# Optimization experiments

Hardware: AMD Instinct MI355X
Metric: run time of the kernel (lower is better)

The kernel has to match this reference:

```python
import jax, jax.numpy as jnp
import numpy as np

B, H, W, C = 16, 32, 32, 512
HEADS, DHEAD = 8, 64  # head * channel == C
GROUPS, EPS = 32, 1e-5


def setup_inputs() -> dict:
    key = jax.random.key(0)
    ks = jax.random.split(key, 6)
    return {
        "x": jax.random.normal(ks[0], (B, H, W, C), jnp.float32),
        "gn_gamma": jnp.ones((C,), jnp.float32),
        "gn_beta": jnp.zeros((C,), jnp.float32),
        "wq": jax.random.normal(ks[1], (C, HEADS * DHEAD), jnp.float32) * 0.02,
        "wk": jax.random.normal(ks[2], (C, HEADS * DHEAD), jnp.float32) * 0.02,
        "wv": jax.random.normal(ks[3], (C, HEADS * DHEAD), jnp.float32) * 0.02,
        "conv_w": jax.random.normal(ks[4], (3, 3, HEADS * DHEAD, C), jnp.float32) * 0.02,
        "conv_b": jnp.zeros((C,), jnp.float32),
    }


def _group_norm(x, gamma, beta):
    b, h, w, c = x.shape
    xg = x.reshape(b, h, w, GROUPS, c // GROUPS)
    mean = jnp.mean(xg, axis=(1, 2, 4), keepdims=True)
    var = jnp.var(xg, axis=(1, 2, 4), keepdims=True)
    xn = (xg - mean) * jax.lax.rsqrt(var + EPS)
    return xn.reshape(b, h, w, c) * gamma + beta


def reference(x, gn_gamma, gn_beta, wq, wk, wv, conv_w, conv_b):
    xn = _group_norm(x, gn_gamma, gn_beta)          # [B,H,W,C]
    t = xn.reshape(B, H * W, C)                      # tokens [B,S,C]
    q = (t @ wq).reshape(B, H * W, HEADS, DHEAD)
    k = (t @ wk).reshape(B, H * W, HEADS, DHEAD)
    v = (t @ wv).reshape(B, H * W, HEADS, DHEAD)
    scale = 1.0 / jnp.sqrt(jnp.asarray(DHEAD, q.dtype))
    scores = jnp.einsum("bqhd,bkhd->bhqk", q, k) * scale  # [B,HEADS,S,S]
    weights = jax.nn.softmax(scores, axis=-1)
    out = jnp.einsum("bhqk,bkhd->bqhd", weights, v)       # [B,S,HEADS,DHEAD]
    out = out.reshape(B, H, W, HEADS * DHEAD)
    y = jax.lax.conv_general_dilated(
        out, conv_w, window_strides=(1, 1), padding=((1, 1), (1, 1)),
        dimension_numbers=("NHWC", "HWIO", "NHWC")) + conv_b
    return y + x
```

## Files before the change

kernel.cpp:

```cpp
#include <hip/hip_runtime.h>
#include <hip/hip_bf16.h>

#define Bn 16
#define Cc 512
#define Ss 1024
#define HEADS 8
#define DHEAD 64
#define GROUPS 32
#define CPG 16
#define EPSv 1e-5f
#define Mtok (Bn*Ss)
#define QKVS 1536
#define PROW 34
#define PIMG (PROW*PROW)

typedef __hip_bfloat16 bf16;
typedef __attribute__((ext_vector_type(8))) short short8;
typedef __attribute__((ext_vector_type(4))) float f32x4;

union U4 { uint4 u; bf16 h[8]; };
union B4 { ushort4 u; bf16 h[4]; };

__device__ __forceinline__ void stage16(const bf16* g, bf16* l) {
    __builtin_amdgcn_global_load_lds((const __attribute__((address_space(1))) void*)g,
                                     (__attribute__((address_space(3))) void*)l,
                                     16, 0, 0);
}

__global__ __launch_bounds__(256) void wtrans(const float* __restrict__ src,
                                              bf16* __restrict__ dst) {
    size_t off = (size_t)blockIdx.y * 262144;
    int t = blockIdx.x * 256 + threadIdx.x;
    int n = t & 511, k8 = (t >> 9) * 8;
    const float* s = src + off + (size_t)k8 * 512 + n;
    U4 o;
#pragma unroll
    for (int j = 0; j < 8; j++) o.h[j] = __float2bfloat16(s[(size_t)j * 512]);
    *(uint4*)(dst + off + (size_t)n * 512 + k8) = o.u;
}

__global__ __launch_bounds__(256) void gn_stats(const float* __restrict__ x,
                                                float* __restrict__ stats) {
    int bg = blockIdx.x;
    int b = bg >> 5, g = bg & 31;
    int tid = threadIdx.x;
    const size_t base = (size_t)b * Ss * Cc + g * CPG;
    float sum = 0.f, sq = 0.f;
    for (int i = tid; i < 4096; i += 256) {
        int s = i >> 2, c4 = (i & 3) * 4;
        float4 t = *(const float4*)(x + base + (size_t)s * Cc + c4);
        sum += t.x + t.y + t.z + t.w;
        sq  += t.x * t.x + t.y * t.y + t.z * t.z + t.w * t.w;
    }
    __shared__ float s1[4], s2[4];
#pragma unroll
    for (int off = 32; off > 0; off >>= 1) {
        sum += __shfl_down(sum, off);
        sq  += __shfl_down(sq,  off);
    }
    if ((tid & 63) == 0) { s1[tid >> 6] = sum; s2[tid >> 6] = sq; }
    __syncthreads();
    if (tid == 0) {
        float S = s1[0] + s1[1] + s1[2] + s1[3];
        float Q = s2[0] + s2[1] + s2[2] + s2[3];
        float mean = S * (1.f / 16384.f);
        float var  = Q * (1.f / 16384.f) - mean * mean;
        stats[bg * 2 + 0] = mean;
        stats[bg * 2 + 1] = rsqrtf(var + EPSv);
    }
}

__global__ __launch_bounds__(256) void gn_apply(const float* __restrict__ x,
                                                const float* __restrict__ stats,
                                                const float* __restrict__ gamma,
                                                const float* __restrict__ beta,
                                                bf16* __restrict__ xn) {
    size_t i = (size_t)blockIdx.x * 256 + threadIdx.x;
    size_t e = i * 4;
    int c0 = (int)(e & (Cc - 1));
    int token = (int)(e >> 9);
    int b = token >> 10;
    int g = c0 >> 4;
    float mean = stats[(b * 32 + g) * 2 + 0];
    float rstd = stats[(b * 32 + g) * 2 + 1];
    float4 t  = *(const float4*)(x + e);
    float4 gm = *(const float4*)(gamma + c0);
    float4 bt = *(const float4*)(beta + c0);
    B4 o;
    o.h[0] = __float2bfloat16((t.x - mean) * rstd * gm.x + bt.x);
    o.h[1] = __float2bfloat16((t.y - mean) * rstd * gm.y + bt.y);
    o.h[2] = __float2bfloat16((t.z - mean) * rstd * gm.z + bt.z);
    o.h[3] = __float2bfloat16((t.w - mean) * rstd * gm.w + bt.w);
    *(ushort4*)(xn + e) = o.u;
}

__global__ __launch_bounds__(256) void zero_pad(bf16* __restrict__ Pad) {
    int idx = blockIdx.x * 256 + threadIdx.x;
    int b = idx / (132 * 64);
    int rem = idx - b * 132 * 64;
    int t = rem >> 6, seg = rem & 63;
    int r, c;
    if (t < 34)      { r = 0;  c = t; }
    else if (t < 68) { r = 33; c = t - 34; }
    else { int u = t - 68; r = 1 + (u >> 1); c = (u & 1) * 33; }
    uint4 z = {0u, 0u, 0u, 0u};
    *(uint4*)(Pad + ((size_t)b * PIMG + r * PROW + c) * Cc + seg * 8) = z;
}

__global__ __launch_bounds__(256) void gemm_qkv(const bf16* __restrict__ A,
                                                const bf16* __restrict__ Wt,
                                                bf16* __restrict__ C) {
    __shared__ __align__(16) bf16 As[128][32];
    __shared__ __align__(16) bf16 Bs[128][32];
    int tid = threadIdx.x;
    int wave = tid >> 6, lane = tid & 63;
    int l15 = lane & 15, quad = lane >> 4;
    int wm = wave >> 1, wn = wave & 1;
    int m0 = blockIdx.y * 128, n0 = blockIdx.x * 128;
    int lr = lane >> 2, kseg = (lane & 3) * 8;
    int ar0 = wave * 32 + lr;

    const bf16* ga = A  + (size_t)(m0 + ar0) * Cc + kseg;
    const bf16* gb = Wt + (size_t)(n0 + ar0) * Cc + kseg;
    bf16* la0 = &As[wave * 32][0];
    bf16* la1 = &As[wave * 32 + 16][0];
    bf16* lb0 = &Bs[wave * 32][0];
    bf16* lb1 = &Bs[wave * 32 + 16][0];

    f32x4 acc[4][4] = {};
    for (int k0 = 0; k0 < 512; k0 += 32) {
        __syncthreads();
        stage16(ga + k0,                  la0);
        stage16(ga + k0 + (size_t)16 * Cc, la1);
        stage16(gb + k0,                  lb0);
        stage16(gb + k0 + (size_t)16 * Cc, lb1);
        __syncthreads();
        short8 af[4], bfv[4];
#pragma unroll
        for (int mt = 0; mt < 4; mt++) af[mt]  = *(const short8*)&As[wm * 64 + mt * 16 + l15][quad * 8];
#pragma unroll
        for (int nt = 0; nt < 4; nt++) bfv[nt] = *(const short8*)&Bs[wn * 64 + nt * 16 + l15][quad * 8];
#pragma unroll
        for (int mt = 0; mt < 4; mt++)
#pragma unroll
            for (int nt = 0; nt < 4; nt++)
                acc[mt][nt] = __builtin_amdgcn_mfma_f32_16x16x32_bf16(af[mt], bfv[nt], acc[mt][nt], 0, 0, 0);
    }
#pragma unroll
    for (int mt = 0; mt < 4; mt++)
#pragma unroll
        for (int r = 0; r < 4; r++) {
            size_t row = (size_t)(m0 + wm * 64 + mt * 16 + quad * 4 + r) * QKVS + n0 + wn * 64 + l15;
#pragma unroll
            for (int nt = 0; nt < 4; nt++)
                C[row + nt * 16] = __float2bfloat16(acc[mt][nt][r]);
        }
}

__global__ __launch_bounds__(256) void attention_mfma(const bf16* __restrict__ QKV,
                                                      bf16* __restrict__ Pad) {
    int blk = blockIdx.x;
    int qt = blk & 15;
    int bh = blk >> 4;
    int h = bh & (HEADS - 1), b = bh >> 3;
    int tid = threadIdx.x;
    int wave = tid >> 6, lane = tid & 63;
    int l15 = lane & 15, quad = lane >> 4;

    __shared__ __align__(16) bf16 Ks[2][32][72];
    __shared__ __align__(16) bf16 Vt[2][64][40];
    __shared__ __align__(16) bf16 Ps[4][16][40];

    const size_t base = (size_t)b * Ss * QKVS + h * DHEAD;
    const bf16* kbase = QKV + base + 512;
    const bf16* vbase = QKV + base + 1024;

    int q0 = qt * 64 + wave * 16;
    const bf16* qrow = QKV + base + (size_t)(q0 + l15) * QKVS + quad * 8;
    short8 qf0 = *(const short8*)(qrow);
    short8 qf1 = *(const short8*)(qrow + 32);

    f32x4 oacc[4] = {{0.f,0.f,0.f,0.f},{0.f,0.f,0.f,0.f},{0.f,0.f,0.f,0.f},{0.f,0.f,0.f,0.f}};
    float lsum[4] = {0.f, 0.f, 0.f, 0.f};
    const f32x4 zero4 = {0.f, 0.f, 0.f, 0.f};

    int tok = tid & 31, d0 = (tid >> 5) * 8;

    uint4 nk, nv;
    {
        const size_t rb = (size_t)tok * QKVS + d0;
        nk = *(const uint4*)(kbase + rb);
        nv = *(const uint4*)(vbase + rb);
    }
    *(uint4*)&Ks[0][tok][d0] = nk;
    { U4 u; u.u = nv;
#pragma unroll
      for (int i = 0; i < 8; i++) Vt[0][d0 + i][tok] = u.h[i]; }
    __syncthreads();

    for (int c = 0; c < 32; ++c) {
        int buf = c & 1;
        if (c + 1 < 32) {
            const size_t rb = (size_t)((c + 1) * 32 + tok) * QKVS + d0;
            nk = *(const uint4*)(kbase + rb);
            nv = *(const uint4*)(vbase + rb);
        }
#pragma unroll
        for (int kg = 0; kg < 2; kg++) {
            short8 kf0 = *(const short8*)&Ks[buf][kg * 16 + l15][quad * 8];
            short8 kf1 = *(const short8*)&Ks[buf][kg * 16 + l15][32 + quad * 8];
            f32x4 s = __builtin_amdgcn_mfma_f32_16x16x32_bf16(qf0, kf0, zero4, 0, 0, 0);
            s = __builtin_amdgcn_mfma_f32_16x16x32_bf16(qf1, kf1, s, 0, 0, 0);
#pragma unroll
            for (int r = 0; r < 4; r++) {
                float p = __expf(s[r] * 0.125f);
                lsum[r] += p;
                Ps[wave][quad * 4 + r][kg * 16 + l15] = __float2bfloat16(p);
            }
        }
        short8 pf = *(const short8*)&Ps[wave][l15][quad * 8];
#pragma unroll
        for (int dt = 0; dt < 4; dt++) {
            short8 vf = *(const short8*)&Vt[buf][dt * 16 + l15][quad * 8];
            oacc[dt] = __builtin_amdgcn_mfma_f32_16x16x32_bf16(pf, vf, oacc[dt], 0, 0, 0);
        }
        if (c + 1 < 32) {
            *(uint4*)&Ks[buf ^ 1][tok][d0] = nk;
            U4 u; u.u = nv;
#pragma unroll
            for (int i = 0; i < 8; i++) Vt[buf ^ 1][d0 + i][tok] = u.h[i];
        }
        __syncthreads();
    }

#pragma unroll
    for (int r = 0; r < 4; r++) {
#pragma unroll
        for (int m = 1; m < 16; m <<= 1) lsum[r] += __shfl_xor(lsum[r], m);
    }
#pragma unroll
    for (int r = 0; r < 4; r++) {
        float inv = 1.f / lsum[r];
        int s = q0 + quad * 4 + r;
        size_t rowoff = ((size_t)(b * PROW + (s >> 5) + 1) * PROW + (s & 31) + 1) * Cc + h * DHEAD;
#pragma unroll
        for (int dt = 0; dt < 4; dt++)
            Pad[rowoff + dt * 16 + l15] = __float2bfloat16(oacc[dt][r] * inv);
    }
}

__global__ __launch_bounds__(256) void conv_mfma(const bf16* __restrict__ Pad,
                                                 const bf16* __restrict__ Wct,
                                                 const float* __restrict__ bias,
                                                 const float* __restrict__ xres,
                                                 float* __restrict__ out) {
    __shared__ __align__(16) bf16 As[128][32];
    __shared__ __align__(16) bf16 Bs[128][32];
    int tid = threadIdx.x;
    int wave = tid >> 6, lane = tid & 63;
    int l15 = lane & 15, quad = lane >> 4;
    int wm = wave >> 1, wn = wave & 1;
    int m0 = blockIdx.y * 128, n0 = blockIdx.x * 128;
    int lr = lane >> 2, kseg = (lane & 3) * 8;
    int ar0 = wave * 32 + lr;

    int tok = m0 + ar0;
    int b = tok >> 10, oh = (tok & 1023) >> 5, ow = tok & 31;
    int prow = (b * PROW + oh + 1) * PROW + ow + 1;

    const bf16* gb = Wct + (size_t)(n0 + ar0) * Cc + kseg;
    bf16* la0 = &As[wave * 32][0];
    bf16* la1 = &As[wave * 32 + 16][0];
    bf16* lb0 = &Bs[wave * 32][0];
    bf16* lb1 = &Bs[wave * 32 + 16][0];

    f32x4 acc[4][4] = {};
    for (int tap = 0; tap < 9; ++tap) {
        int dy = tap / 3 - 1, dx = tap % 3 - 1;
        const bf16* ga = Pad + (size_t)(prow + dy * PROW + dx) * Cc + kseg;
        const bf16* gw = gb + (size_t)tap * (Cc * Cc);
        for (int k0 = 0; k0 < 512; k0 += 32) {
            __syncthreads();
            stage16(ga + k0,                   la0);
            stage16(ga + k0 + (size_t)16 * Cc, la1);
            stage16(gw + k0,                   lb0);
            stage16(gw + k0 + (size_t)16 * Cc, lb1);
            __syncthreads();
            short8 af[4], bfv[4];
#pragma unroll
            for (int mt = 0; mt < 4; mt++) af[mt]  = *(const short8*)&As[wm * 64 + mt * 16 + l15][quad * 8];
#pragma unroll
            for (int nt = 0; nt < 4; nt++) bfv[nt] = *(const short8*)&Bs[wn * 64 + nt * 16 + l15][quad * 8];
#pragma unroll
            for (int mt = 0; mt < 4; mt++)
#pragma unroll
                for (int nt = 0; nt < 4; nt++)
                    acc[mt][nt] = __builtin_amdgcn_mfma_f32_16x16x32_bf16(af[mt], bfv[nt], acc[mt][nt], 0, 0, 0);
        }
    }
#pragma unroll
    for (int mt = 0; mt < 4; mt++)
#pragma unroll
        for (int r = 0; r < 4; r++) {
            size_t row = (size_t)(m0 + wm * 64 + mt * 16 + quad * 4 + r) * Cc + n0 + wn * 64 + l15;
#pragma unroll
            for (int nt = 0; nt < 4; nt++) {
                int n = n0 + wn * 64 + nt * 16 + l15;
                out[row + nt * 16] = acc[mt][nt][r] + bias[n] + xres[row + nt * 16];
            }
        }
}

extern "C" void kernel_launch(void* const* d_in, const int* in_sizes, int n_in,
                              void* d_out, int out_size, void* d_ws, size_t ws_size,
                              hipStream_t stream) {
    const float* x     = (const float*)d_in[0];
    const float* gamma = (const float*)d_in[1];
    const float* beta  = (const float*)d_in[2];
    const float* wq    = (const float*)d_in[3];
    const float* wk    = (const float*)d_in[4];
    const float* wv    = (const float*)d_in[5];
    const float* convw = (const float*)d_in[6];
    const float* convb = (const float*)d_in[7];
    float* out = (float*)d_out;

    char* ws = (char*)d_ws;
    bf16*  pad   = (bf16*)ws;
    float* stats = (float*)ws;
    bf16*  xn    = (bf16*)(ws + 4096);
    bf16*  wt    = (bf16*)(ws + 4096 + ((size_t)16 << 20));
    bf16*  qkv   = (bf16*)(ws + ((size_t)19 << 20));
    bf16*  wct   = (bf16*)(ws + ((size_t)67 << 20));

    wtrans<<<dim3(128, 1), 256, 0, stream>>>(wq, wt);
    wtrans<<<dim3(128, 1), 256, 0, stream>>>(wk, wt + 262144);
    wtrans<<<dim3(128, 1), 256, 0, stream>>>(wv, wt + 524288);
    wtrans<<<dim3(128, 9), 256, 0, stream>>>(convw, wct);

    gn_stats<<<dim3(Bn * GROUPS), 256, 0, stream>>>(x, stats);
    gn_apply<<<dim3(Mtok * Cc / (4 * 256)), 256, 0, stream>>>(x, stats, gamma, beta, xn);

    gemm_qkv<<<dim3(QKVS / 128, Mtok / 128), 256, 0, stream>>>(xn, wt, qkv);

    zero_pad<<<dim3(528), 256, 0, stream>>>(pad);
    attention_mfma<<<dim3(Bn * HEADS * (Ss / 64)), 256, 0, stream>>>(qkv, pad);

    conv_mfma<<<dim3(Cc / 128, Mtok / 128), 256, 0, stream>>>(pad, wct, convb, x, out);
}
```

Measured before the change: 353.6 us.

## Split QKV output into separate Q/K and transposed V buffers, swizzle GEMM block order

The QKV GEMM now writes Q and K to separate token-major buffers and writes V transposed (channel-major per batch), so attention can read V fragments straight from global memory instead of transposing them through LDS. The attention loop drops the register-prefetch double buffering and stages 64-key K tiles into LDS once per step. Both GEMM and conv kernels use a 1D grid with a remapped block index so that neighbouring blocks share M rows and weight tiles in cache. The trade-off is uncoalesced-ish global V reads inside the inner loop, and the loss of overlap between K loads and compute.

```diff
diff --git a/kernel.cpp b/kernel.cpp
--- a/kernel.cpp
+++ b/kernel.cpp
@@ -10,7 +10,6 @@
 #define CPG 16
 #define EPSv 1e-5f
 #define Mtok (Bn*Ss)
-#define QKVS 1536
 #define PROW 34
 #define PIMG (PROW*PROW)
 
@@ -109,14 +108,20 @@
 
 __global__ __launch_bounds__(256) void gemm_qkv(const bf16* __restrict__ A,
                                                 const bf16* __restrict__ Wt,
-                                                bf16* __restrict__ C) {
+                                                bf16* __restrict__ qbuf,
+                                                bf16* __restrict__ kbuf,
+                                                bf16* __restrict__ vt) {
+    int id = blockIdx.x;
+    int m_blk = ((id & 7) << 4) + ((id >> 3) & 15);
+    int n_blk = id >> 7;
+    int m0 = m_blk * 128, n0 = n_blk * 128;
+
     __shared__ __align__(16) bf16 As[128][32];
     __shared__ __align__(16) bf16 Bs[128][32];
     int tid = threadIdx.x;
     int wave = tid >> 6, lane = tid & 63;
     int l15 = lane & 15, quad = lane >> 4;
     int wm = wave >> 1, wn = wave & 1;
-    int m0 = blockIdx.y * 128, n0 = blockIdx.x * 128;
     int lr = lane >> 2, kseg = (lane & 3) * 8;
     int ar0 = wave * 32 + lr;
 
@@ -130,9 +135,9 @@
     f32x4 acc[4][4] = {};
     for (int k0 = 0; k0 < 512; k0 += 32) {
         __syncthreads();
-        stage16(ga + k0,                  la0);
+        stage16(ga + k0,                   la0);
         stage16(ga + k0 + (size_t)16 * Cc, la1);
-        stage16(gb + k0,                  lb0);
+        stage16(gb + k0,                   lb0);
         stage16(gb + k0 + (size_t)16 * Cc, lb1);
         __syncthreads();
         short8 af[4], bfv[4];
@@ -146,18 +151,40 @@
             for (int nt = 0; nt < 4; nt++)
                 acc[mt][nt] = __builtin_amdgcn_mfma_f32_16x16x32_bf16(af[mt], bfv[nt], acc[mt][nt], 0, 0, 0);
     }
-#pragma unroll
-    for (int mt = 0; mt < 4; mt++)
-#pragma unroll
-        for (int r = 0; r < 4; r++) {
-            size_t row = (size_t)(m0 + wm * 64 + mt * 16 + quad * 4 + r) * QKVS + n0 + wn * 64 + l15;
-#pragma unroll
-            for (int nt = 0; nt < 4; nt++)
-                C[row + nt * 16] = __float2bfloat16(acc[mt][nt][r]);
-        }
-}
-
-__global__ __launch_bounds__(256) void attention_mfma(const bf16* __restrict__ QKV,
+
+    int nbase = n0 + wn * 64;
+    if (n0 < 1024) {
+        bf16* dst = (n0 < 512) ? qbuf : kbuf;
+        int nn = nbase & 511;
+#pragma unroll
+        for (int mt = 0; mt < 4; mt++)
+#pragma unroll
+            for (int r = 0; r < 4; r++) {
+                size_t row = (size_t)(m0 + wm * 64 + mt * 16 + quad * 4 + r) * Cc + nn + l15;
+#pragma unroll
+                for (int nt = 0; nt < 4; nt++)
+                    dst[row + nt * 16] = __float2bfloat16(acc[mt][nt][r]);
+            }
+    } else {
+        int b = m0 >> 10;
+        int tok0 = (m0 & 1023) + wm * 64;
+#pragma unroll
+        for (int mt = 0; mt < 4; mt++)
+#pragma unroll
+            for (int nt = 0; nt < 4; nt++) {
+                int cch = (nbase - 1024) + nt * 16 + l15;
+                B4 o;
+#pragma unroll
+                for (int r = 0; r < 4; r++) o.h[r] = __float2bfloat16(acc[mt][nt][r]);
+                *(ushort4*)(vt + (size_t)b * 524288 + (size_t)cch * 1024
+                               + tok0 + mt * 16 + quad * 4) = o.u;
+            }
+    }
+}
+
+__global__ __launch_bounds__(256) void attention_mfma(const bf16* __restrict__ qbuf,
+                                                      const bf16* __restrict__ kbuf,
+                                                      const bf16* __restrict__ vt,
                                                       bf16* __restrict__ Pad) {
     int blk = blockIdx.x;
     int qt = blk & 15;
@@ -167,16 +194,14 @@
     int wave = tid >> 6, lane = tid & 63;
     int l15 = lane & 15, quad = lane >> 4;
 
-    __shared__ __align__(16) bf16 Ks[2][32][72];
-    __shared__ __align__(16) bf16 Vt[2][64][40];
+    __shared__ __align__(16) bf16 Ks[64][72];
     __shared__ __align__(16) bf16 Ps[4][16][40];
 
-    const size_t base = (size_t)b * Ss * QKVS + h * DHEAD;
-    const bf16* kbase = QKV + base + 512;
-    const bf16* vbase = QKV + base + 1024;
+    const bf16* kb = kbuf + (size_t)b * Ss * Cc + h * DHEAD;
+    const bf16* vb = vt + (size_t)b * 524288 + (size_t)h * DHEAD * Ss;
 
     int q0 = qt * 64 + wave * 16;
-    const bf16* qrow = QKV + base + (size_t)(q0 + l15) * QKVS + quad * 8;
+    const bf16* qrow = qbuf + ((size_t)b * Ss + q0 + l15) * Cc + h * DHEAD + quad * 8;
     short8 qf0 = *(const short8*)(qrow);
     short8 qf1 = *(const short8*)(qrow + 32);
 
@@ -184,53 +209,40 @@
     float lsum[4] = {0.f, 0.f, 0.f, 0.f};
     const f32x4 zero4 = {0.f, 0.f, 0.f, 0.f};
 
-    int tok = tid & 31, d0 = (tid >> 5) * 8;
-
-    uint4 nk, nv;
-    {
-        const size_t rb = (size_t)tok * QKVS + d0;
-        nk = *(const uint4*)(kbase + rb);
-        nv = *(const uint4*)(vbase + rb);
-    }
-    *(uint4*)&Ks[0][tok][d0] = nk;
-    { U4 u; u.u = nv;
-#pragma unroll
-      for (int i = 0; i < 8; i++) Vt[0][d0 + i][tok] = u.h[i]; }
-    __syncthreads();
-
-    for (int c = 0; c < 32; ++c) {
-        int buf = c & 1;
-        if (c + 1 < 32) {
-            const size_t rb = (size_t)((c + 1) * 32 + tok) * QKVS + d0;
-            nk = *(const uint4*)(kbase + rb);
-            nv = *(const uint4*)(vbase + rb);
+    int t0 = tid * 2;
+    int tokA = t0 >> 3, segA = (t0 & 7) * 8;
+    int tokB = tokA,    segB = ((t0 + 1) & 7) * 8;
+
+    for (int c = 0; c < 16; ++c) {
+        __syncthreads();
+        const bf16* kc = kb + (size_t)(c * 64) * Cc;
+        *(uint4*)&Ks[tokA][segA] = *(const uint4*)(kc + (size_t)tokA * Cc + segA);
+        *(uint4*)&Ks[tokB][segB] = *(const uint4*)(kc + (size_t)tokB * Cc + segB);
+        __syncthreads();
+#pragma unroll
+        for (int kp = 0; kp < 2; ++kp) {
+#pragma unroll
+            for (int kh = 0; kh < 2; ++kh) {
+                int kg = kp * 2 + kh;
+                short8 kf0 = *(const short8*)&Ks[kg * 16 + l15][quad * 8];
+                short8 kf1 = *(const short8*)&Ks[kg * 16 + l15][32 + quad * 8];
+                f32x4 s = __builtin_amdgcn_mfma_f32_16x16x32_bf16(qf0, kf0, zero4, 0, 0, 0);
+                s = __builtin_amdgcn_mfma_f32_16x16x32_bf16(qf1, kf1, s, 0, 0, 0);
+#pragma unroll
+                for (int r = 0; r < 4; r++) {
+                    float p = __expf(s[r] * 0.125f);
+                    lsum[r] += p;
+                    Ps[wave][quad * 4 + r][kh * 16 + l15] = __float2bfloat16(p);
+                }
+            }
+            short8 pf = *(const short8*)&Ps[wave][l15][quad * 8];
+            const bf16* vsub = vb + c * 64 + kp * 32 + quad * 8;
+#pragma unroll
+            for (int dt = 0; dt < 4; dt++) {
+                short8 vf = *(const short8*)(vsub + (size_t)(dt * 16 + l15) * Ss);
+                oacc[dt] = __builtin_amdgcn_mfma_f32_16x16x32_bf16(pf, vf, oacc[dt], 0, 0, 0);
+            }
         }
-#pragma unroll
-        for (int kg = 0; kg < 2; kg++) {
-            short8 kf0 = *(const short8*)&Ks[buf][kg * 16 + l15][quad * 8];
-            short8 kf1 = *(const short8*)&Ks[buf][kg * 16 + l15][32 + quad * 8];
-            f32x4 s = __builtin_amdgcn_mfma_f32_16x16x32_bf16(qf0, kf0, zero4, 0, 0, 0);
-            s = __builtin_amdgcn_mfma_f32_16x16x32_bf16(qf1, kf1, s, 0, 0, 0);
-#pragma unroll
-            for (int r = 0; r < 4; r++) {
-                float p = __expf(s[r] * 0.125f);
-                lsum[r] += p;
-                Ps[wave][quad * 4 + r][kg * 16 + l15] = __float2bfloat16(p);
-            }
-        }
-        short8 pf = *(const short8*)&Ps[wave][l15][quad * 8];
-#pragma unroll
-        for (int dt = 0; dt < 4; dt++) {
-            short8 vf = *(const short8*)&Vt[buf][dt * 16 + l15][quad * 8];
-            oacc[dt] = __builtin_amdgcn_mfma_f32_16x16x32_bf16(pf, vf, oacc[dt], 0, 0, 0);
-        }
-        if (c + 1 < 32) {
-            *(uint4*)&Ks[buf ^ 1][tok][d0] = nk;
-            U4 u; u.u = nv;
-#pragma unroll
-            for (int i = 0; i < 8; i++) Vt[buf ^ 1][d0 + i][tok] = u.h[i];
-        }
-        __syncthreads();
     }
 
 #pragma unroll
@@ -254,13 +266,17 @@
                                                  const float* __restrict__ bias,
                                                  const float* __restrict__ xres,
                                                  float* __restrict__ out) {
+    int id = blockIdx.x;
+    int m_blk = ((id & 7) << 4) + ((id >> 3) & 15);
+    int n_blk = id >> 7;
+    int m0 = m_blk * 128, n0 = n_blk * 128;
+
     __shared__ __align__(16) bf16 As[128][32];
     __shared__ __align__(16) bf16 Bs[128][32];
     int tid = threadIdx.x;
     int wave = tid >> 6, lane = tid & 63;
     int l15 = lane & 15, quad = lane >> 4;
     int wm = wave >> 1, wn = wave & 1;
-    int m0 = blockIdx.y * 128, n0 = blockIdx.x * 128;
     int lr = lane >> 2, kseg = (lane & 3) * 8;
     int ar0 = wave * 32 + lr;
 
@@ -329,7 +345,9 @@
     float* stats = (float*)ws;
     bf16*  xn    = (bf16*)(ws + 4096);
     bf16*  wt    = (bf16*)(ws + 4096 + ((size_t)16 << 20));
-    bf16*  qkv   = (bf16*)(ws + ((size_t)19 << 20));
+    bf16*  qbuf  = (bf16*)(ws + ((size_t)19 << 20));
+    bf16*  kbuf  = (bf16*)(ws + ((size_t)35 << 20));
+    bf16*  vt    = (bf16*)(ws + ((size_t)51 << 20));
     bf16*  wct   = (bf16*)(ws + ((size_t)67 << 20));
 
     wtrans<<<dim3(128, 1), 256, 0, stream>>>(wq, wt);
@@ -340,10 +358,10 @@
     gn_stats<<<dim3(Bn * GROUPS), 256, 0, stream>>>(x, stats);
     gn_apply<<<dim3(Mtok * Cc / (4 * 256)), 256, 0, stream>>>(x, stats, gamma, beta, xn);
 
-    gemm_qkv<<<dim3(QKVS / 128, Mtok / 128), 256, 0, stream>>>(xn, wt, qkv);
+    gemm_qkv<<<dim3(1536), 256, 0, stream>>>(xn, wt, qbuf, kbuf, vt);
 
     zero_pad<<<dim3(528), 256, 0, stream>>>(pad);
-    attention_mfma<<<dim3(Bn * HEADS * (Ss / 64)), 256, 0, stream>>>(qkv, pad);
-
-    conv_mfma<<<dim3(Cc / 128, Mtok / 128), 256, 0, stream>>>(pad, wct, convb, x, out);
-}
+    attention_mfma<<<dim3(Bn * HEADS * (Ss / 64)), 256, 0, stream>>>(qbuf, kbuf, vt, pad);
+
+    conv_mfma<<<dim3(512), 256, 0, stream>>>(pad, wct, convb, x, out);
+}
```

After: 385.1 us. +8.9%, slower.
